# Optimization experiments

Measured on AMD Instinct MI355X. Metric: run time of the kernel, lower is better.

Reference implementation:

```python
import jax, jax.numpy as jnp
import numpy as np

D_MODEL = 1024
N_HEADS = 16
N_GROUPS = 4
CONTEXT_LEN = 512
D_H = D_MODEL // N_HEADS          # 64
GROUP_SIZE = N_HEADS // N_GROUPS  # 4
B, S = 4, 2048


def setup_inputs() -> dict:
    key = jax.random.key(0)
    ks = jax.random.split(key, 9)
    s = 0.02
    return {
        "x": jax.random.normal(ks[0], (B, S, D_MODEL), dtype=jnp.float32),
        "Wq": jax.random.normal(ks[1], (D_MODEL, D_MODEL), dtype=jnp.float32) * s,
        "bq": jax.random.normal(ks[2], (D_MODEL,), dtype=jnp.float32) * s,
        "Wk": jax.random.normal(ks[3], (D_MODEL, N_GROUPS * D_H), dtype=jnp.float32) * s,
        "bk": jax.random.normal(ks[4], (N_GROUPS * D_H,), dtype=jnp.float32) * s,
        "Wv": jax.random.normal(ks[5], (D_MODEL, N_GROUPS * D_H), dtype=jnp.float32) * s,
        "bv": jax.random.normal(ks[6], (N_GROUPS * D_H,), dtype=jnp.float32) * s,
        "Wo": jax.random.normal(ks[7], (D_MODEL, D_MODEL), dtype=jnp.float32) * s,
        "bo": jax.random.normal(ks[8], (D_MODEL,), dtype=jnp.float32) * s,
    }


def reference(x, Wq, bq, Wk, bk, Wv, bv, Wo, bo):
    b, s = x.shape[0], x.shape[1]
    # Projections. q: [b, n_groups, group_size, s, d_h]; k/v: [b, n_groups, s, d_h]
    q = (x @ Wq + bq).reshape(b, s, N_GROUPS, GROUP_SIZE, D_H)
    q = jnp.transpose(q, (0, 2, 3, 1, 4))
    k = jnp.transpose((x @ Wk + bk).reshape(b, s, N_GROUPS, D_H), (0, 2, 1, 3))
    v = jnp.transpose((x @ Wv + bv).reshape(b, s, N_GROUPS, D_H), (0, 2, 1, 3))
    # Grouped scores (einsum broadcast == repeat_interleave of k over group_size)
    scores = jnp.einsum("bghqd,bgkd->bghqk", q, k) / jnp.sqrt(jnp.float32(D_H))
    # Sliding-window causal mask (cached_len == s when use_cache=False)
    i = jnp.arange(s)
    j = jnp.arange(s)
    upper = (i - CONTEXT_LEN)[:, None] >= j[None, :]   # too-old keys
    lower = i[:, None] < j[None, :]                    # future keys
    mask = upper | lower                               # [s, s]
    scores = jnp.where(mask, jnp.float32(-1e9), scores)
    att = jax.nn.softmax(scores, axis=-1)
    out = jnp.einsum("bghqk,bgkd->bghqd", att, v)      # [b, g, h, s, d_h]
    out = jnp.transpose(out, (0, 3, 1, 2, 4)).reshape(b, s, D_MODEL)
    return out @ Wo + bo
```

## Files before the change

### kernel.cpp

```cpp
#include <hip/hip_runtime.h>
#include <cstdint>
#include <cstddef>

typedef __attribute__((ext_vector_type(8))) short short8;
typedef __attribute__((ext_vector_type(4))) short short4v;
typedef __attribute__((ext_vector_type(4))) float f32x4;
typedef __attribute__((ext_vector_type(4))) unsigned short ushort4v;
typedef unsigned short ushort_t;

union Frag8 { short4v h[2]; short8 v; };
union PFrag { unsigned int w[4]; short8 v; };

__device__ __forceinline__ ushort_t f2bf(float f) {
  unsigned int u = __builtin_bit_cast(unsigned int, f);
  u += 0x7FFFu + ((u >> 16) & 1u);
  return (ushort_t)(u >> 16);
}

__device__ __forceinline__ void gload16(const void* g, void* l) {
  __builtin_amdgcn_global_load_lds(
      (const __attribute__((address_space(1))) unsigned int*)g,
      (__attribute__((address_space(3))) unsigned int*)l, 16, 0, 0);
}

__global__ void cast_x_kernel(const float* __restrict__ x, ushort_t* __restrict__ o) {
  int i = (blockIdx.x * 256 + threadIdx.x) * 4;
  const float4 v = *reinterpret_cast<const float4*>(x + i);
  ushort4v r = { f2bf(v.x), f2bf(v.y), f2bf(v.z), f2bf(v.w) };
  *reinterpret_cast<ushort4v*>(o + i) = r;
}

__global__ __launch_bounds__(256) void transpose_w_kernel(
    const float* __restrict__ Wq, const float* __restrict__ Wk,
    const float* __restrict__ Wv, const float* __restrict__ Wo,
    ushort_t* __restrict__ Wt) {
  __shared__ float tile[32][33];
  const int tn = blockIdx.x, tk = blockIdx.y;
  const int n0 = tn * 32;
  const float* W; int ldn, nloc;
  if      (n0 < 1024) { W = Wq; ldn = 1024; nloc = n0; }
  else if (n0 < 1280) { W = Wk; ldn = 256;  nloc = n0 - 1024; }
  else if (n0 < 1536) { W = Wv; ldn = 256;  nloc = n0 - 1280; }
  else                { W = Wo; ldn = 1024; nloc = n0 - 1536; }
  const int t = threadIdx.x;
  const int sr = t >> 3, sc = (t & 7) * 4;
  const float4 v = *reinterpret_cast<const float4*>(W + (size_t)(tk * 32 + sr) * ldn + nloc + sc);
  tile[sr][sc] = v.x; tile[sr][sc + 1] = v.y; tile[sr][sc + 2] = v.z; tile[sr][sc + 3] = v.w;
  __syncthreads();
  const int wr = t >> 3, wc = (t & 7) * 4;
  ushort4v o = { f2bf(tile[wc][wr]), f2bf(tile[wc + 1][wr]),
                 f2bf(tile[wc + 2][wr]), f2bf(tile[wc + 3][wr]) };
  *reinterpret_cast<ushort4v*>(Wt + (size_t)(n0 + wr) * 1024 + tk * 32 + wc) = o;
}

__global__ void prep_bias_kernel(const float* __restrict__ bq, const float* __restrict__ bk,
                                 const float* __restrict__ bv, float* __restrict__ bqkv) {
  int t = blockIdx.x * 256 + threadIdx.x;
  if (t < 1536) bqkv[t] = (t < 1024) ? bq[t] : (t < 1280) ? bk[t - 1024] : bv[t - 1280];
}

#define GEMM_IDS \
  const int tid = threadIdx.x;                        \
  const int w = tid >> 6, lane = tid & 63;            \
  const int wm = w >> 1, wn = w & 1;                  \
  const int g = lane >> 4, r16 = lane & 15;

#define GEMM_KLOOP(APTR, BPTR)                                                          \
  const f32x4 vzero = {0.f, 0.f, 0.f, 0.f};                                             \
  f32x4 acc[8][4];                                                                      \
  _Pragma("unroll") for (int i = 0; i < 8; ++i)                                         \
    _Pragma("unroll") for (int j = 0; j < 4; ++j) acc[i][j] = vzero;                    \
  const int su = (lane & 3) ^ ((lane >> 3) & 3);                                        \
  const int sr = lane >> 2;                                                             \
  auto stage = [&](int s, int k0) {                                                     \
    char* base = LdsB + s * 24576;                                                      \
    _Pragma("unroll") for (int i = 0; i < 4; ++i) {                                     \
      const int c = w * 4 + i;                                                          \
      gload16((const char*)(APTR) + (size_t)(bm * 256 + c * 16 + sr) * 2048 + k0 * 2 + su * 16, \
              base + c * 1024);                                                         \
    }                                                                                   \
    _Pragma("unroll") for (int i = 0; i < 2; ++i) {                                     \
      const int c = w * 2 + i;                                                          \
      gload16((const char*)(BPTR) + (size_t)(bn * 128 + c * 16 + sr) * 2048 + k0 * 2 + su * 16, \
              base + 16384 + c * 1024);                                                 \
    }                                                                                   \
  };                                                                                    \
  stage(0, 0);                                                                          \
  stage(1, 32);                                                                         \
  const int fsw = (g ^ ((r16 >> 1) & 3)) << 4;                                          \
  for (int t = 0; t < 32; ++t) {                                                        \
    if (t < 31) { asm volatile("s_waitcnt vmcnt(6) lgkmcnt(0)" ::: "memory"); }         \
    else        { asm volatile("s_waitcnt vmcnt(0) lgkmcnt(0)" ::: "memory"); }         \
    __builtin_amdgcn_s_barrier();                                                       \
    if (t + 2 < 32) stage((t + 2) % 3, (t + 2) * 32);                                   \
    const char* Ab = LdsB + (t % 3) * 24576;                                            \
    const char* Bb = Ab + 16384;                                                        \
    short8 af[8], bf[4];                                                                \
    _Pragma("unroll") for (int mi = 0; mi < 8; ++mi)                                    \
      af[mi] = *(const short8*)(Ab + (wm * 128 + mi * 16 + r16) * 64 + fsw);            \
    _Pragma("unroll") for (int ni = 0; ni < 4; ++ni)                                    \
      bf[ni] = *(const short8*)(Bb + (wn * 64 + ni * 16 + r16) * 64 + fsw);             \
    __builtin_amdgcn_s_setprio(1);                                                      \
    _Pragma("unroll") for (int mi = 0; mi < 8; ++mi)                                    \
      _Pragma("unroll") for (int ni = 0; ni < 4; ++ni)                                  \
        acc[mi][ni] = __builtin_amdgcn_mfma_f32_16x16x32_bf16(af[mi], bf[ni], acc[mi][ni], 0, 0, 0); \
    __builtin_amdgcn_s_setprio(0);                                                      \
  }

__global__ __launch_bounds__(256, 2) void gemm_qkv_kernel(
    const ushort_t* __restrict__ A, const ushort_t* __restrict__ Bt,
    const float* __restrict__ bias,
    ushort_t* __restrict__ Qb, ushort_t* __restrict__ Kb, ushort_t* __restrict__ Vt)
{
  __shared__ __align__(16) char LdsB[73728];
  const int xcd = blockIdx.x & 7, ii = blockIdx.x >> 3;
  const int bm = xcd * 4 + ii / 12, bn = ii % 12;
  GEMM_IDS
  GEMM_KLOOP(A, Bt)

  float bcol[4];
#pragma unroll
  for (int ni = 0; ni < 4; ++ni) bcol[ni] = bias[bn * 128 + wn * 64 + ni * 16 + r16];
  if (bn < 8) {
#pragma unroll
    for (int mi = 0; mi < 8; ++mi)
#pragma unroll
      for (int ni = 0; ni < 4; ++ni) {
        const int col = bn * 128 + wn * 64 + ni * 16 + r16;
#pragma unroll
        for (int rr = 0; rr < 4; ++rr) {
          const int row = bm * 256 + wm * 128 + mi * 16 + g * 4 + rr;
          Qb[(size_t)row * 1024 + col] = f2bf(acc[mi][ni][rr] + bcol[ni]);
        }
      }
  } else if (bn < 10) {
#pragma unroll
    for (int mi = 0; mi < 8; ++mi)
#pragma unroll
      for (int ni = 0; ni < 4; ++ni) {
        const int c = bn * 128 + wn * 64 + ni * 16 + r16 - 1024;
        const int gi = c >> 6, dd = c & 63;
#pragma unroll
        for (int rr = 0; rr < 4; ++rr) {
          const int row = bm * 256 + wm * 128 + mi * 16 + g * 4 + rr;
          const int bb = row >> 11, s = row & 2047;
          Kb[((size_t)(bb * 4 + gi) * 2048 + s) * 64 + dd] = f2bf(acc[mi][ni][rr] + bcol[ni]);
        }
      }
  } else {
#pragma unroll
    for (int mi = 0; mi < 8; ++mi) {
      const int row0 = bm * 256 + wm * 128 + mi * 16 + g * 4;
      const int bb = row0 >> 11, s0 = row0 & 2047;
#pragma unroll
      for (int ni = 0; ni < 4; ++ni) {
        const int c = bn * 128 + wn * 64 + ni * 16 + r16 - 1280;
        const int gi = c >> 6, dd = c & 63;
        ushort4v pk;
#pragma unroll
        for (int rr = 0; rr < 4; ++rr) pk[rr] = f2bf(acc[mi][ni][rr] + bcol[ni]);
        *reinterpret_cast<ushort4v*>(Vt + ((size_t)(bb * 4 + gi) * 64 + dd) * 2048 + s0) = pk;
      }
    }
  }
}

__global__ __launch_bounds__(256, 2) void gemm_out_kernel(
    const ushort_t* __restrict__ A, const ushort_t* __restrict__ Bt,
    const float* __restrict__ bias, float* __restrict__ Cout)
{
  __shared__ __align__(16) char LdsB[73728];
  const int xcd = blockIdx.x & 7, ii = blockIdx.x >> 3;
  const int bm = xcd * 4 + (ii >> 3), bn = ii & 7;
  GEMM_IDS
  GEMM_KLOOP(A, Bt)

  float bcol[4];
#pragma unroll
  for (int ni = 0; ni < 4; ++ni) bcol[ni] = bias[bn * 128 + wn * 64 + ni * 16 + r16];
#pragma unroll
  for (int mi = 0; mi < 8; ++mi)
#pragma unroll
    for (int ni = 0; ni < 4; ++ni) {
      const int col = bn * 128 + wn * 64 + ni * 16 + r16;
#pragma unroll
      for (int rr = 0; rr < 4; ++rr) {
        const int row = bm * 256 + wm * 128 + mi * 16 + g * 4 + rr;
        Cout[(size_t)row * 1024 + col] = acc[mi][ni][rr] + bcol[ni];
      }
    }
}

__global__ __launch_bounds__(512, 2) void attn_kernel(
    const ushort_t* __restrict__ Qb, const ushort_t* __restrict__ Kb,
    const ushort_t* __restrict__ Vt, ushort_t* __restrict__ attout)
{
  __shared__ __align__(16) char KsB[16384];
  __shared__ __align__(16) char VsB[16384];
  const int fid = blockIdx.x + 32 * (blockIdx.y + 4 * blockIdx.z);
  const int j = fid >> 3;
  const int qt = (fid & 7) * 4 + (j >> 4);
  const int gg = j & 3, b = (j >> 2) & 3;

  const int tid = threadIdx.x;
  const int w = tid >> 6, lane = tid & 63;
  const int hw = w & 3, qh = w >> 2;
  const int h = gg * 4 + hw;
  const int g = lane >> 4, r16 = lane & 15;
  const int u0 = g >> 1;
  const int lowb = (g & 1) << 3;
  const int q0w = qt * 64 + qh * 32;

  short8 qf[2][2];
#pragma unroll
  for (int qs = 0; qs < 2; ++qs) {
    const char* qptr = (const char*)Qb + ((size_t)(b * 2048 + q0w + qs * 16 + r16) * 1024 + h * 64) * 2;
#pragma unroll
    for (int dc = 0; dc < 2; ++dc)
      qf[qs][dc] = *(const short8*)(qptr + dc * 64 + g * 16);
  }

  const f32x4 vzero = {0.f, 0.f, 0.f, 0.f};
  f32x4 accO[2][4];
#pragma unroll
  for (int qs = 0; qs < 2; ++qs)
#pragma unroll
    for (int nt = 0; nt < 4; ++nt) accO[qs][nt] = vzero;
  float lsum[2] = {0.f, 0.f};

  const char* KbB = (const char*)Kb + (size_t)(b * 4 + gg) * 2048 * 128;
  const char* VtB = (const char*)Vt + (size_t)(b * 4 + gg) * 64 * 4096;

  const int kb0 = (qt >= 8) ? (qt * 64 - 512) : 0;
  const int NT = (qt * 64 + 64 - kb0) >> 6;

  const int srr = tid >> 3, spk = tid & 7;
  auto stage = [&](int buf, int kb) {
    gload16(KbB + (size_t)(kb + srr) * 128 + ((spk ^ (srr & 7)) << 4),
            KsB + buf * 8192 + tid * 16);
    gload16(VtB + (size_t)srr * 4096 + (size_t)kb * 2 + ((spk ^ (srr & 7)) << 4),
            VsB + buf * 8192 + tid * 16);
  };

  stage(0, kb0);
  __syncthreads();
  for (int t = 0; t < NT; ++t) {
    const int kb = kb0 + t * 64;
    const int cur = t & 1;
    if (t + 1 < NT) stage(cur ^ 1, kb + 64);
    const char* Ks = KsB + cur * 8192;
    const char* Vs = VsB + cur * 8192;
    const bool full = (kb >= q0w - 480) && (kb <= q0w - 63);

    f32x4 st[2][4];
#pragma unroll
    for (int ki = 0; ki < 4; ++ki) {
      const int key = ki * 16 + r16;
      const int swz = key & 7;
      const short8 kf0 = *(const short8*)(Ks + key * 128 + ((g ^ swz) << 4));
      const short8 kf1 = *(const short8*)(Ks + key * 128 + (((4 + g) ^ swz) << 4));
#pragma unroll
      for (int qs = 0; qs < 2; ++qs) {
        st[qs][ki] = __builtin_amdgcn_mfma_f32_16x16x32_bf16(kf0, qf[qs][0], vzero, 0, 0, 0);
        st[qs][ki] = __builtin_amdgcn_mfma_f32_16x16x32_bf16(kf1, qf[qs][1], st[qs][ki], 0, 0, 0);
      }
    }

    PFrag pf[2][2];
#pragma unroll
    for (int qs = 0; qs < 2; ++qs) {
      const int q = q0w + qs * 16 + r16;
#pragma unroll
      for (int ki = 0; ki < 4; ++ki)
#pragma unroll
        for (int r = 0; r < 4; ++r) {
          float s = st[qs][ki][r] * 0.180336881f;
          if (!full) {
            const int key = kb + ki * 16 + g * 4 + r;
            const bool valid = (key <= q) && (key + 512 > q);
            s = valid ? s : -INFINITY;
          }
          st[qs][ki][r] = __builtin_amdgcn_exp2f(s);
        }
      float tk[4];
#pragma unroll
      for (int ki = 0; ki < 4; ++ki)
        tk[ki] = (st[qs][ki][0] + st[qs][ki][1]) + (st[qs][ki][2] + st[qs][ki][3]);
      lsum[qs] += (tk[0] + tk[1]) + (tk[2] + tk[3]);
#pragma unroll
      for (int c = 0; c < 2; ++c)
#pragma unroll
        for (int pr = 0; pr < 2; ++pr) {
          asm("v_cvt_pk_bf16_f32 %0, %1, %2"
              : "=v"(pf[qs][c].w[pr * 2])
              : "v"(st[qs][2 * c + pr][0]), "v"(st[qs][2 * c + pr][1]));
          asm("v_cvt_pk_bf16_f32 %0, %1, %2"
              : "=v"(pf[qs][c].w[pr * 2 + 1])
              : "v"(st[qs][2 * c + pr][2]), "v"(st[qs][2 * c + pr][3]));
        }
    }

#pragma unroll
    for (int c = 0; c < 2; ++c)
#pragma unroll
      for (int nt = 0; nt < 4; ++nt) {
        const int d = nt * 16 + r16;
        const int swz = d & 7;
        Frag8 vf;
        vf.h[0] = *(const short4v*)(Vs + d * 128 + (((c * 4 + u0) ^ swz) << 4) + lowb);
        vf.h[1] = *(const short4v*)(Vs + d * 128 + (((c * 4 + 2 + u0) ^ swz) << 4) + lowb);
#pragma unroll
        for (int qs = 0; qs < 2; ++qs)
          accO[qs][nt] = __builtin_amdgcn_mfma_f32_16x16x32_bf16(pf[qs][c].v, vf.v, accO[qs][nt], 0, 0, 0);
      }
    __syncthreads();
  }

#pragma unroll
  for (int qs = 0; qs < 2; ++qs) {
    float ts = lsum[qs];
    ts += __shfl_xor(ts, 16);
    ts += __shfl_xor(ts, 32);
    const float linv = 1.f / ts;
    float lq[4];
#pragma unroll
    for (int rr = 0; rr < 4; ++rr) lq[rr] = __shfl(linv, g * 4 + rr);
#pragma unroll
    for (int nt = 0; nt < 4; ++nt) {
      const int ocol = h * 64 + nt * 16 + r16;
#pragma unroll
      for (int rr = 0; rr < 4; ++rr) {
        const int orow = b * 2048 + q0w + qs * 16 + g * 4 + rr;
        attout[(size_t)orow * 1024 + ocol] = f2bf(accO[qs][nt][rr] * lq[rr]);
      }
    }
  }
}

extern "C" void kernel_launch(void* const* d_in, const int* in_sizes, int n_in,
                              void* d_out, int out_size, void* d_ws, size_t ws_size,
                              hipStream_t stream) {
  (void)in_sizes; (void)n_in; (void)out_size; (void)ws_size;
  const float* x  = (const float*)d_in[0];
  const float* Wq = (const float*)d_in[1];
  const float* bq = (const float*)d_in[2];
  const float* Wk = (const float*)d_in[3];
  const float* bk = (const float*)d_in[4];
  const float* Wv = (const float*)d_in[5];
  const float* bv = (const float*)d_in[6];
  const float* Wo = (const float*)d_in[7];
  const float* bo = (const float*)d_in[8];

  char* ws = (char*)d_ws;
  ushort_t* Qb   = (ushort_t*)(ws + 0);
  ushort_t* Kb   = (ushort_t*)(ws + 16777216);
  ushort_t* Vt   = (ushort_t*)(ws + 20971520);
  ushort_t* wt   = (ushort_t*)(ws + 25165824);
  float*    bqkv = (float*)   (ws + 30408704);
  ushort_t* xb   = (ushort_t*)(ws + 30416896);
  ushort_t* att  = (ushort_t*)(ws + 47194112);

  cast_x_kernel<<<8192, 256, 0, stream>>>(x, xb);
  transpose_w_kernel<<<dim3(80, 32), 256, 0, stream>>>(Wq, Wk, Wv, Wo, wt);
  prep_bias_kernel<<<6, 256, 0, stream>>>(bq, bk, bv, bqkv);
  gemm_qkv_kernel<<<384, 256, 0, stream>>>(xb, wt, bqkv, Qb, Kb, Vt);
  attn_kernel<<<dim3(32, 4, 4), 512, 0, stream>>>(Qb, Kb, Vt, att);
  gemm_out_kernel<<<256, 256, 0, stream>>>(att, wt + (size_t)1536 * 1024, bo, (float*)d_out);
}
```

Baseline: 118.7 us.

## Triple-buffer attention K/V, prescale Q, permute V layout for single-load fragments

The attention loop moves from double to triple buffering, with explicit vmcnt waits and a single barrier per iteration, so global-to-LDS loads run two tiles ahead. The softmax scale is folded into Q in the QKV GEMM epilogue, which removes a multiply per score. V is stored with permuted sequence positions so each PV fragment comes from one 16-byte LDS read instead of two 8-byte reads. The grid is flattened and processes the longest query tiles first for better load balance. The cost is more LDS per block and a layout dependency between the two kernels.

```diff
diff --git a/kernel.cpp b/kernel.cpp
--- a/kernel.cpp
+++ b/kernel.cpp
@@ -130,7 +130,7 @@
 #pragma unroll
         for (int rr = 0; rr < 4; ++rr) {
           const int row = bm * 256 + wm * 128 + mi * 16 + g * 4 + rr;
-          Qb[(size_t)row * 1024 + col] = f2bf(acc[mi][ni][rr] + bcol[ni]);
+          Qb[(size_t)row * 1024 + col] = f2bf((acc[mi][ni][rr] + bcol[ni]) * 0.180336881f);
         }
       }
   } else if (bn < 10) {
@@ -151,7 +151,9 @@
 #pragma unroll
     for (int mi = 0; mi < 8; ++mi) {
       const int row0 = bm * 256 + wm * 128 + mi * 16 + g * 4;
-      const int bb = row0 >> 11, s0 = row0 & 2047;
+      const int bb = row0 >> 11;
+      const int s = row0 & 2047;
+      const int pos = (s & ~31) + g * 8 + (mi & 1) * 4;
 #pragma unroll
       for (int ni = 0; ni < 4; ++ni) {
         const int c = bn * 128 + wn * 64 + ni * 16 + r16 - 1280;
@@ -159,7 +161,7 @@
         ushort4v pk;
 #pragma unroll
         for (int rr = 0; rr < 4; ++rr) pk[rr] = f2bf(acc[mi][ni][rr] + bcol[ni]);
-        *reinterpret_cast<ushort4v*>(Vt + ((size_t)(bb * 4 + gi) * 64 + dd) * 2048 + s0) = pk;
+        *reinterpret_cast<ushort4v*>(Vt + ((size_t)(bb * 4 + gi) * 64 + dd) * 2048 + pos) = pk;
       }
     }
   }
@@ -195,20 +197,19 @@
     const ushort_t* __restrict__ Qb, const ushort_t* __restrict__ Kb,
     const ushort_t* __restrict__ Vt, ushort_t* __restrict__ attout)
 {
-  __shared__ __align__(16) char KsB[16384];
-  __shared__ __align__(16) char VsB[16384];
-  const int fid = blockIdx.x + 32 * (blockIdx.y + 4 * blockIdx.z);
-  const int j = fid >> 3;
-  const int qt = (fid & 7) * 4 + (j >> 4);
-  const int gg = j & 3, b = (j >> 2) & 3;
+  __shared__ __align__(16) char KsB[24576];
+  __shared__ __align__(16) char VsB[24576];
+  const int fid = blockIdx.x;
+  const int lo = fid & 7, hi = fid >> 3;
+  const int qt = 31 - (hi & 31);
+  const int gbsel = lo | ((hi >> 5) << 3);
+  const int gg = gbsel & 3, b = gbsel >> 2;
 
   const int tid = threadIdx.x;
   const int w = tid >> 6, lane = tid & 63;
   const int hw = w & 3, qh = w >> 2;
   const int h = gg * 4 + hw;
   const int g = lane >> 4, r16 = lane & 15;
-  const int u0 = g >> 1;
-  const int lowb = (g & 1) << 3;
   const int q0w = qt * 64 + qh * 32;
 
   short8 qf[2][2];
@@ -243,14 +244,15 @@
   };
 
   stage(0, kb0);
-  __syncthreads();
+  if (NT > 1) stage(1, kb0 + 64);
   for (int t = 0; t < NT; ++t) {
+    if (t < NT - 1) { asm volatile("s_waitcnt vmcnt(2) lgkmcnt(0)" ::: "memory"); }
+    else            { asm volatile("s_waitcnt vmcnt(0) lgkmcnt(0)" ::: "memory"); }
+    __builtin_amdgcn_s_barrier();
+    if (t + 2 < NT) stage((t + 2) % 3, kb0 + (t + 2) * 64);
     const int kb = kb0 + t * 64;
-    const int cur = t & 1;
-    if (t + 1 < NT) stage(cur ^ 1, kb + 64);
-    const char* Ks = KsB + cur * 8192;
-    const char* Vs = VsB + cur * 8192;
-    const bool full = (kb >= q0w - 480) && (kb <= q0w - 63);
+    const char* Ks = KsB + (t % 3) * 8192;
+    const char* Vs = VsB + (t % 3) * 8192;
 
     f32x4 st[2][4];
 #pragma unroll
@@ -266,22 +268,33 @@
       }
     }
 
+    const bool full = (kb >= q0w - 480) && (kb <= q0w - 63);
     PFrag pf[2][2];
-#pragma unroll
-    for (int qs = 0; qs < 2; ++qs) {
-      const int q = q0w + qs * 16 + r16;
-#pragma unroll
-      for (int ki = 0; ki < 4; ++ki)
-#pragma unroll
-        for (int r = 0; r < 4; ++r) {
-          float s = st[qs][ki][r] * 0.180336881f;
-          if (!full) {
+    if (full) {
+#pragma unroll
+      for (int qs = 0; qs < 2; ++qs) {
+#pragma unroll
+        for (int ki = 0; ki < 4; ++ki)
+#pragma unroll
+          for (int r = 0; r < 4; ++r)
+            st[qs][ki][r] = __builtin_amdgcn_exp2f(st[qs][ki][r]);
+      }
+    } else {
+#pragma unroll
+      for (int qs = 0; qs < 2; ++qs) {
+        const int q = q0w + qs * 16 + r16;
+#pragma unroll
+        for (int ki = 0; ki < 4; ++ki)
+#pragma unroll
+          for (int r = 0; r < 4; ++r) {
             const int key = kb + ki * 16 + g * 4 + r;
             const bool valid = (key <= q) && (key + 512 > q);
-            s = valid ? s : -INFINITY;
+            st[qs][ki][r] = __builtin_amdgcn_exp2f(valid ? st[qs][ki][r] : -INFINITY);
           }
-          st[qs][ki][r] = __builtin_amdgcn_exp2f(s);
-        }
+      }
+    }
+#pragma unroll
+    for (int qs = 0; qs < 2; ++qs) {
       float tk[4];
 #pragma unroll
       for (int ki = 0; ki < 4; ++ki)
@@ -305,15 +318,11 @@
 #pragma unroll
       for (int nt = 0; nt < 4; ++nt) {
         const int d = nt * 16 + r16;
-        const int swz = d & 7;
-        Frag8 vf;
-        vf.h[0] = *(const short4v*)(Vs + d * 128 + (((c * 4 + u0) ^ swz) << 4) + lowb);
-        vf.h[1] = *(const short4v*)(Vs + d * 128 + (((c * 4 + 2 + u0) ^ swz) << 4) + lowb);
+        const short8 vf = *(const short8*)(Vs + d * 128 + (((c * 4 + g) ^ (d & 7)) << 4));
 #pragma unroll
         for (int qs = 0; qs < 2; ++qs)
-          accO[qs][nt] = __builtin_amdgcn_mfma_f32_16x16x32_bf16(pf[qs][c].v, vf.v, accO[qs][nt], 0, 0, 0);
-      }
-    __syncthreads();
+          accO[qs][nt] = __builtin_amdgcn_mfma_f32_16x16x32_bf16(pf[qs][c].v, vf, accO[qs][nt], 0, 0, 0);
+      }
   }
 
 #pragma unroll
@@ -364,6 +373,6 @@
   transpose_w_kernel<<<dim3(80, 32), 256, 0, stream>>>(Wq, Wk, Wv, Wo, wt);
   prep_bias_kernel<<<6, 256, 0, stream>>>(bq, bk, bv, bqkv);
   gemm_qkv_kernel<<<384, 256, 0, stream>>>(xb, wt, bqkv, Qb, Kb, Vt);
-  attn_kernel<<<dim3(32, 4, 4), 512, 0, stream>>>(Qb, Kb, Vt, att);
+  attn_kernel<<<512, 512, 0, stream>>>(Qb, Kb, Vt, att);
   gemm_out_kernel<<<256, 256, 0, stream>>>(att, wt + (size_t)1536 * 1024, bo, (float*)d_out);
 }
```

Result: faster. 105.8 us (-10.9%).
